# Kernel optimization log

Hardware: AMD Instinct MI355X
Metric: run time of the kernel (lower is better)

## Reference

```python
import jax, jax.numpy as jnp
import numpy as np

B, T, C = 32, 1024, 512
COND_CH = 256            # = L + 4
L = COND_CH - 4          # raw cond length
RES = 64
S = 2 * RES              # kv sequence length
LN_EPS = 1e-5


def _layernorm(x, w, b):
    mu = jnp.mean(x, axis=-1, keepdims=True)
    var = jnp.var(x, axis=-1, keepdims=True)
    return (x - mu) * jax.lax.rsqrt(var + LN_EPS) * w + b


def setup_inputs() -> dict:
    key = jax.random.key(0)
    ks = jax.random.split(key, 12)
    sc = 0.02
    return {
        "x": jax.random.normal(ks[0], (B, T, C), dtype=jnp.float32),
        "cond_emb": jax.random.normal(ks[1], (B, 1, L), dtype=jnp.float32),
        "Wq": sc * jax.random.normal(ks[2], (C, C), dtype=jnp.float32),
        "bq": jnp.zeros((C,), jnp.float32),
        "Wk": sc * jax.random.normal(ks[3], (C, COND_CH), dtype=jnp.float32),
        "bk": jnp.zeros((C,), jnp.float32),
        "Wv": sc * jax.random.normal(ks[4], (C, COND_CH), dtype=jnp.float32),
        "bv": jnp.zeros((C,), jnp.float32),
        "conv_w": sc * jax.random.normal(ks[5], (S, 1, 1), dtype=jnp.float32),
        "conv_b": jnp.zeros((S,), jnp.float32),
        "ln1_w": jnp.ones((C,), jnp.float32),
        "ln1_b": jnp.zeros((C,), jnp.float32),
        "W1": sc * jax.random.normal(ks[6], (2 * C, C), dtype=jnp.float32),
        "b1": jnp.zeros((2 * C,), jnp.float32),
        "W2": sc * jax.random.normal(ks[7], (C, 2 * C), dtype=jnp.float32),
        "b2": jnp.zeros((C,), jnp.float32),
        "ln2_w": jnp.ones((C,), jnp.float32),
        "ln2_b": jnp.zeros((C,), jnp.float32),
    }


def reference(x, cond_emb, Wq, bq, Wk, bk, Wv, bv, conv_w, conv_b,
              ln1_w, ln1_b, W1, b1, W2, b2, ln2_w, ln2_b):
    # conditioner_projection: Conv1d(1, 2*RES, k=1, padding=2, circular)
    # circular pad last dim by 2 on each side -> length L+4 == COND_CH
    pad = jnp.pad(cond_emb, ((0, 0), (0, 0), (2, 2)), mode="wrap")   # [B,1,L+4]
    cond = conv_w.reshape(1, S, 1) * pad + conv_b.reshape(1, S, 1)    # [B,S,L+4]

    q = x @ Wq.T + bq                 # [B,T,C]
    k = cond @ Wk.T + bk              # [B,S,C]
    v = cond @ Wv.T + bv              # [B,S,C]

    scale = 1.0 / jnp.sqrt(jnp.float32(C))
    scores = jnp.einsum("btc,bsc->bts", q, k) * scale   # [B,T,S]
    attn = jax.nn.softmax(scores, axis=-1)
    attn_out = jnp.einsum("bts,bsc->btc", attn, v)       # [B,T,C]

    query = _layernorm(q + attn_out, ln1_w, ln1_b)
    h = jax.nn.gelu(query @ W1.T + b1, approximate=False)
    ff = h @ W2.T + b2
    out = _layernorm(query + ff, ln2_w, ln2_b)
    return out + x
```

## Files before the change

### kernel.cpp

```cpp
#include <hip/hip_runtime.h>
#include <hip/hip_bf16.h>
#include <cstdint>


typedef __attribute__((ext_vector_type(8))) short bf16x8;
typedef __attribute__((ext_vector_type(4))) float f32x4;
typedef __attribute__((ext_vector_type(8))) unsigned short u16x8;

__device__ __forceinline__ float bf2f(unsigned short u) {
  union { unsigned int i; float f; } x; x.i = ((unsigned int)u) << 16; return x.f;
}
__device__ __forceinline__ unsigned short f2bf(float f) {
  unsigned int u = __float_as_uint(f);
  unsigned int r = (u + 0x7FFFu + ((u >> 16) & 1u)) >> 16;
  return (unsigned short)r;
}

__device__ __forceinline__ float wave_sum(float v) {
#pragma unroll
  for (int m = 1; m < 64; m <<= 1) v += __shfl_xor(v, m, 64);
  return v;
}
__device__ __forceinline__ float wave_max(float v) {
#pragma unroll
  for (int m = 1; m < 64; m <<= 1) v = fmaxf(v, __shfl_xor(v, m, 64));
  return v;
}

template <int F32>
__device__ __forceinline__ void stage16(const void* base, size_t eoff,
                                        unsigned short* dst) {
  if (F32) {
    const float* s = (const float*)base + eoff;
    f32x4 a0 = *(const f32x4*)s, a1 = *(const f32x4*)(s + 4);
    u16x8 t;
#pragma unroll
    for (int j = 0; j < 4; ++j) { t[j] = f2bf(a0[j]); t[j + 4] = f2bf(a1[j]); }
    *(u16x8*)dst = t;
  } else {
    *(u16x8*)dst = *(const u16x8*)((const unsigned short*)base + eoff);
  }
}

__global__ __launch_bounds__(256) void prep(
    const float* __restrict__ cond_emb,
    const float* __restrict__ Wk,
    const float* __restrict__ Wv,
    float* __restrict__ Ak, float* __restrict__ Av,
    float* __restrict__ Wks, float* __restrict__ Wvs) {
  const int t = blockIdx.x * 256 + threadIdx.x;
  const int b = t >> 9, c = t & 511;
  const float* ce = cond_emb + b * 252;
  float ak = 0.f, av = 0.f, ks = 0.f, vs = 0.f;
  for (int i = 0; i < 256; ++i) {
    int idx = i - 2; if (idx < 0) idx += 252; if (idx >= 252) idx -= 252;
    float p = ce[idx];
    float wk = Wk[c * 256 + i];
    float wv = Wv[c * 256 + i];
    ak += p * wk; av += p * wv; ks += wk; vs += wv;
  }
  Ak[b * 512 + c] = ak;
  Av[b * 512 + c] = av;
  if (b == 0) { Wks[c] = ks; Wvs[c] = vs; }
}

template <int EPI, int AF32, int BF32>
__global__ __launch_bounds__(256) void gemm_bt(
    const void* __restrict__ Aptr, const void* __restrict__ Bptr,
    const float* __restrict__ bias, unsigned short* __restrict__ Cc,
    int M, int N, int K) {
  __shared__ __align__(16) unsigned short lds_a[128 * 64];
  __shared__ __align__(16) unsigned short lds_b[128 * 64];
  const int nblk = N >> 7;
  const int bm = (int)blockIdx.x / nblk;
  const int bn = (int)blockIdx.x % nblk;
  const int tid = threadIdx.x;
  const int wave = tid >> 6;
  const int lane = tid & 63;
  const int wm = (wave >> 1) << 6;
  const int wn = (wave & 1) << 6;
  const int quad = lane >> 4;
  const int l16 = lane & 15;
  const int srow = lane >> 3;
  const int scol = (lane & 7) << 3;

  f32x4 acc[4][4] = {};

  const size_t abase = (size_t)(bm * 128) * (size_t)K;
  const size_t bbase = (size_t)(bn * 128) * (size_t)K;

  for (int k0 = 0; k0 < K; k0 += 64) {
#pragma unroll
    for (int j = 0; j < 4; ++j) {
      const int rr = wave * 32 + j * 8 + srow;
      stage16<AF32>(Aptr, abase + (size_t)rr * K + (k0 + scol), &lds_a[rr * 64 + scol]);
      stage16<BF32>(Bptr, bbase + (size_t)rr * K + (k0 + scol), &lds_b[rr * 64 + scol]);
    }
    __syncthreads();
#pragma unroll
    for (int kk = 0; kk < 64; kk += 32) {
      bf16x8 af[4], bfr[4];
#pragma unroll
      for (int i = 0; i < 4; ++i)
        af[i] = *(const bf16x8*)&lds_a[(wm + i * 16 + l16) * 64 + kk + quad * 8];
#pragma unroll
      for (int i = 0; i < 4; ++i)
        bfr[i] = *(const bf16x8*)&lds_b[(wn + i * 16 + l16) * 64 + kk + quad * 8];
#pragma unroll
      for (int mi = 0; mi < 4; ++mi)
#pragma unroll
        for (int ni = 0; ni < 4; ++ni)
          acc[mi][ni] = __builtin_amdgcn_mfma_f32_16x16x32_bf16(
              af[mi], bfr[ni], acc[mi][ni], 0, 0, 0);
    }
    __syncthreads();
  }

#pragma unroll
  for (int ni = 0; ni < 4; ++ni) {
    const int col = bn * 128 + wn + ni * 16 + l16;
    const float bsv = bias[col];
#pragma unroll
    for (int mi = 0; mi < 4; ++mi) {
#pragma unroll
      for (int r = 0; r < 4; ++r) {
        const int row = bm * 128 + wm + mi * 16 + quad * 4 + r;
        float v = acc[mi][ni][r] + bsv;
        if (EPI == 1) v = 0.5f * v * (1.0f + erff(v * 0.70710678118654752f));
        Cc[(size_t)row * N + col] = f2bf(v);
      }
    }
  }
}

__global__ __launch_bounds__(256) void attn_ln(
    unsigned short* qbuf,
    const float* __restrict__ Ak, const float* __restrict__ Av,
    const float* __restrict__ Wks, const float* __restrict__ Wvs,
    const float* __restrict__ bk, const float* __restrict__ bv,
    const float* __restrict__ conv_w, const float* __restrict__ conv_b,
    const float* __restrict__ ln1w, const float* __restrict__ ln1b) {
  const int row = (int)((blockIdx.x * 256 + threadIdx.x) >> 6);
  const int lane = threadIdx.x & 63;
  const int b = row >> 10;
  const int c0 = lane << 3;

  const u16x8 qv = *(const u16x8*)(qbuf + (size_t)row * 512 + c0);
  float qf[8];
#pragma unroll
  for (int j = 0; j < 8; ++j) qf[j] = bf2f(qv[j]);

  const f32x4* akp = (const f32x4*)(Ak + b * 512 + c0);
  const f32x4* avp = (const f32x4*)(Av + b * 512 + c0);
  const f32x4* ksp = (const f32x4*)(Wks + c0);
  const f32x4* vsp = (const f32x4*)(Wvs + c0);
  const f32x4* bkp = (const f32x4*)(bk + c0);
  const f32x4* bvp = (const f32x4*)(bv + c0);
  f32x4 ak0 = akp[0], ak1 = akp[1];
  f32x4 av0 = avp[0], av1 = avp[1];
  f32x4 ks0 = ksp[0], ks1 = ksp[1];
  f32x4 vs0 = vsp[0], vs1 = vsp[1];
  f32x4 bk0 = bkp[0], bk1 = bkp[1];
  f32x4 bv0 = bvp[0], bv1 = bvp[1];

  float u = 0.f, w = 0.f, z = 0.f;
#pragma unroll
  for (int j = 0; j < 8; ++j) {
    float a = (j < 4) ? ak0[j] : ak1[j - 4];
    float s = (j < 4) ? ks0[j] : ks1[j - 4];
    float bb = (j < 4) ? bk0[j] : bk1[j - 4];
    u += qf[j] * a;
    w += qf[j] * s;
    z += qf[j] * bb;
  }
  u = wave_sum(u); w = wave_sum(w); z = wave_sum(z);

  const float scale = 0.044194173824159216f;
  const float cw0 = conv_w[lane], cw1 = conv_w[lane + 64];
  const float cb0 = conv_b[lane], cb1 = conv_b[lane + 64];
  float s0 = scale * (cw0 * u + cb0 * w + z);
  float s1 = scale * (cw1 * u + cb1 * w + z);
  float mx = wave_max(fmaxf(s0, s1));
  float e0 = __expf(s0 - mx), e1 = __expf(s1 - mx);
  float se = wave_sum(e0 + e1);
  float sw = wave_sum(e0 * cw0 + e1 * cw1);
  float sb = wave_sum(e0 * cb0 + e1 * cb1);
  float alpha = sw / se, beta = sb / se;

  float y[8], sy = 0.f, syy = 0.f;
#pragma unroll
  for (int j = 0; j < 8; ++j) {
    float a = (j < 4) ? av0[j] : av1[j - 4];
    float s = (j < 4) ? vs0[j] : vs1[j - 4];
    float bb = (j < 4) ? bv0[j] : bv1[j - 4];
    y[j] = qf[j] + alpha * a + beta * s + bb;
    sy += y[j]; syy += y[j] * y[j];
  }
  sy = wave_sum(sy); syy = wave_sum(syy);
  float mu = sy * (1.0f / 512.0f);
  float var = syy * (1.0f / 512.0f) - mu * mu;
  float rstd = rsqrtf(var + 1e-5f);

  const f32x4* wp = (const f32x4*)(ln1w + c0);
  const f32x4* bp = (const f32x4*)(ln1b + c0);
  f32x4 w0 = wp[0], w1 = wp[1];
  f32x4 b0 = bp[0], b1 = bp[1];
  u16x8 outv;
#pragma unroll
  for (int j = 0; j < 8; ++j) {
    float ww = (j < 4) ? w0[j] : w1[j - 4];
    float bb = (j < 4) ? b0[j] : b1[j - 4];
    outv[j] = f2bf((y[j] - mu) * rstd * ww + bb);
  }
  *(u16x8*)(qbuf + (size_t)row * 512 + c0) = outv;
}

__global__ __launch_bounds__(256) void ln2_res(
    const unsigned short* __restrict__ query,
    const unsigned short* __restrict__ ff,
    const float* __restrict__ x,
    const float* __restrict__ ln2w, const float* __restrict__ ln2b,
    float* __restrict__ out) {
  const int row = (int)((blockIdx.x * 256 + threadIdx.x) >> 6);
  const int lane = threadIdx.x & 63;
  const int c0 = lane << 3;
  const size_t off = (size_t)row * 512 + c0;

  const u16x8 qv = *(const u16x8*)(query + off);
  const u16x8 fv = *(const u16x8*)(ff + off);
  const f32x4* xp = (const f32x4*)(x + off);
  f32x4 x0 = xp[0], x1 = xp[1];
  float y[8], sy = 0.f, syy = 0.f;
#pragma unroll
  for (int j = 0; j < 8; ++j) {
    y[j] = bf2f(qv[j]) + bf2f(fv[j]);
    sy += y[j]; syy += y[j] * y[j];
  }
  sy = wave_sum(sy); syy = wave_sum(syy);
  float mu = sy * (1.0f / 512.0f);
  float var = syy * (1.0f / 512.0f) - mu * mu;
  float rstd = rsqrtf(var + 1e-5f);

  const f32x4* wp = (const f32x4*)(ln2w + c0);
  const f32x4* bp = (const f32x4*)(ln2b + c0);
  f32x4 w0 = wp[0], w1 = wp[1];
  f32x4 b0 = bp[0], b1 = bp[1];
  f32x4 o0, o1;
#pragma unroll
  for (int j = 0; j < 4; ++j) {
    o0[j] = (y[j] - mu) * rstd * w0[j] + b0[j] + x0[j];
    o1[j] = (y[j + 4] - mu) * rstd * w1[j] + b1[j] + x1[j];
  }
  *(f32x4*)(out + off) = o0;
  *(f32x4*)(out + off + 4) = o1;
}


extern "C" void kernel_launch(void* const* d_in, const int* in_sizes, int n_in,
                              void* d_out, int out_size, void* d_ws, size_t ws_size,
                              hipStream_t stream) {
  const float* x        = (const float*)d_in[0];
  const float* cond_emb = (const float*)d_in[1];
  const float* Wq       = (const float*)d_in[2];
  const float* bq       = (const float*)d_in[3];
  const float* Wk       = (const float*)d_in[4];
  const float* bk       = (const float*)d_in[5];
  const float* Wv       = (const float*)d_in[6];
  const float* bv       = (const float*)d_in[7];
  const float* conv_w   = (const float*)d_in[8];
  const float* conv_b   = (const float*)d_in[9];
  const float* ln1w     = (const float*)d_in[10];
  const float* ln1b     = (const float*)d_in[11];
  const float* W1       = (const float*)d_in[12];
  const float* b1       = (const float*)d_in[13];
  const float* W2       = (const float*)d_in[14];
  const float* b2       = (const float*)d_in[15];
  const float* ln2w     = (const float*)d_in[16];
  const float* ln2b     = (const float*)d_in[17];
  float* out = (float*)d_out;

  const int M = 32768;

  char* ws = (char*)d_ws;
  float* Ak  = (float*)(ws);
  float* Av  = (float*)(ws + 65536);
  float* Wks = (float*)(ws + 131072);
  float* Wvs = (float*)(ws + 135168);
  const size_t qoff = (size_t)1 << 20;
  const size_t qbytes = (size_t)M * 512 * 2;
  unsigned short* qbuf = (unsigned short*)(ws + qoff);

  int nc = 1;
  while (nc < 256) {
    size_t need = qoff + qbytes + (size_t)(M / nc) * 3072;
    if (need <= ws_size) break;
    nc <<= 1;
  }
  const int Mc = M / nc;
  unsigned short* hbuf  = (unsigned short*)(ws + qoff + qbytes);
  unsigned short* ffbuf = (unsigned short*)(ws + qoff + qbytes + (size_t)Mc * 2048);

  prep<<<64, 256, 0, stream>>>(cond_emb, Wk, Wv, Ak, Av, Wks, Wvs);

  gemm_bt<0, 1, 1><<<(M / 128) * (512 / 128), 256, 0, stream>>>(
      (const void*)x, (const void*)Wq, bq, qbuf, M, 512, 512);

  attn_ln<<<M / 4, 256, 0, stream>>>(qbuf, Ak, Av, Wks, Wvs, bk, bv,
                                     conv_w, conv_b, ln1w, ln1b);

  for (int c = 0; c < nc; ++c) {
    const size_t roff = (size_t)c * Mc;
    gemm_bt<1, 0, 1><<<(Mc / 128) * (1024 / 128), 256, 0, stream>>>(
        (const void*)(qbuf + roff * 512), (const void*)W1, b1, hbuf, Mc, 1024, 512);
    gemm_bt<0, 0, 1><<<(Mc / 128) * (512 / 128), 256, 0, stream>>>(
        (const void*)hbuf, (const void*)W2, b2, ffbuf, Mc, 512, 1024);
    ln2_res<<<Mc / 4, 256, 0, stream>>>(qbuf + roff * 512, ffbuf, x + roff * 512,
                                        ln2w, ln2b, out + roff * 512);
  }
}
```

Before: 468.7 us.

## Pre-convert weights and x to bf16, stage GEMM tiles via async global-to-LDS loads

Adds a conversion kernel that casts Wq, W1, W2 (and x when workspace allows) to bf16 once per call. The GEMMs then stage bf16 tiles with global_load_lds direct-to-LDS copies instead of register round-trips with per-element fp32-to-bf16 conversion. The prep kernel is also vectorised with float4 weight loads. This removes repeated weight conversion in every GEMM tile, but adds extra passes over x and the weights plus more workspace use.

```diff
diff --git a/kernel.cpp b/kernel.cpp
--- a/kernel.cpp
+++ b/kernel.cpp
@@ -6,6 +6,7 @@
 typedef __attribute__((ext_vector_type(8))) short bf16x8;
 typedef __attribute__((ext_vector_type(4))) float f32x4;
 typedef __attribute__((ext_vector_type(8))) unsigned short u16x8;
+typedef __attribute__((ext_vector_type(4))) unsigned short u16x4;
 
 __device__ __forceinline__ float bf2f(unsigned short u) {
   union { unsigned int i; float f; } x; x.i = ((unsigned int)u) << 16; return x.f;
@@ -27,19 +28,20 @@
   return v;
 }
 
-template <int F32>
-__device__ __forceinline__ void stage16(const void* base, size_t eoff,
-                                        unsigned short* dst) {
-  if (F32) {
-    const float* s = (const float*)base + eoff;
-    f32x4 a0 = *(const f32x4*)s, a1 = *(const f32x4*)(s + 4);
-    u16x8 t;
-#pragma unroll
-    for (int j = 0; j < 4; ++j) { t[j] = f2bf(a0[j]); t[j + 4] = f2bf(a1[j]); }
-    *(u16x8*)dst = t;
-  } else {
-    *(u16x8*)dst = *(const u16x8*)((const unsigned short*)base + eoff);
-  }
+__device__ __forceinline__ void async16(const void* g, void* l) {
+  __builtin_amdgcn_global_load_lds(
+      (const __attribute__((address_space(1))) void*)g,
+      (__attribute__((address_space(3))) void*)l, 16, 0, 0);
+}
+
+__global__ __launch_bounds__(256) void cvt(
+    const float* __restrict__ in, unsigned short* __restrict__ o) {
+  const int i = (blockIdx.x * 256 + threadIdx.x) * 4;
+  f32x4 v = *(const f32x4*)(in + i);
+  u16x4 t;
+#pragma unroll
+  for (int j = 0; j < 4; ++j) t[j] = f2bf(v[j]);
+  *(u16x4*)(o + i) = t;
 }
 
 __global__ __launch_bounds__(256) void prep(
@@ -52,21 +54,24 @@
   const int b = t >> 9, c = t & 511;
   const float* ce = cond_emb + b * 252;
   float ak = 0.f, av = 0.f, ks = 0.f, vs = 0.f;
-  for (int i = 0; i < 256; ++i) {
-    int idx = i - 2; if (idx < 0) idx += 252; if (idx >= 252) idx -= 252;
-    float p = ce[idx];
-    float wk = Wk[c * 256 + i];
-    float wv = Wv[c * 256 + i];
-    ak += p * wk; av += p * wv; ks += wk; vs += wv;
+  for (int i = 0; i < 256; i += 4) {
+    f32x4 wk = *(const f32x4*)(Wk + c * 256 + i);
+    f32x4 wv = *(const f32x4*)(Wv + c * 256 + i);
+#pragma unroll
+    for (int j = 0; j < 4; ++j) {
+      int idx = i + j - 2; if (idx < 0) idx += 252; if (idx >= 252) idx -= 252;
+      float p = ce[idx];
+      ak += p * wk[j]; av += p * wv[j]; ks += wk[j]; vs += wv[j];
+    }
   }
   Ak[b * 512 + c] = ak;
   Av[b * 512 + c] = av;
   if (b == 0) { Wks[c] = ks; Wvs[c] = vs; }
 }
 
-template <int EPI, int AF32, int BF32>
+template <int EPI, int AF32>
 __global__ __launch_bounds__(256) void gemm_bt(
-    const void* __restrict__ Aptr, const void* __restrict__ Bptr,
+    const void* __restrict__ Aptr, const unsigned short* __restrict__ Bm,
     const float* __restrict__ bias, unsigned short* __restrict__ Cc,
     int M, int N, int K) {
   __shared__ __align__(16) unsigned short lds_a[128 * 64];
@@ -92,9 +97,19 @@
   for (int k0 = 0; k0 < K; k0 += 64) {
 #pragma unroll
     for (int j = 0; j < 4; ++j) {
-      const int rr = wave * 32 + j * 8 + srow;
-      stage16<AF32>(Aptr, abase + (size_t)rr * K + (k0 + scol), &lds_a[rr * 64 + scol]);
-      stage16<BF32>(Bptr, bbase + (size_t)rr * K + (k0 + scol), &lds_b[rr * 64 + scol]);
+      const int r = wave * 32 + j * 8;
+      if (AF32) {
+        const float* src = (const float*)Aptr + abase + (size_t)(r + srow) * K + (k0 + scol);
+        f32x4 a0 = *(const f32x4*)src, a1 = *(const f32x4*)(src + 4);
+        u16x8 tv;
+#pragma unroll
+        for (int jj = 0; jj < 4; ++jj) { tv[jj] = f2bf(a0[jj]); tv[jj + 4] = f2bf(a1[jj]); }
+        *(u16x8*)&lds_a[(r + srow) * 64 + scol] = tv;
+      } else {
+        async16((const unsigned short*)Aptr + abase + (size_t)(r + srow) * K + (k0 + scol),
+                &lds_a[r * 64]);
+      }
+      async16(Bm + bbase + (size_t)(r + srow) * K + (k0 + scol), &lds_b[r * 64]);
     }
     __syncthreads();
 #pragma unroll
@@ -169,9 +184,7 @@
     float a = (j < 4) ? ak0[j] : ak1[j - 4];
     float s = (j < 4) ? ks0[j] : ks1[j - 4];
     float bb = (j < 4) ? bk0[j] : bk1[j - 4];
-    u += qf[j] * a;
-    w += qf[j] * s;
-    z += qf[j] * bb;
+    u += qf[j] * a; w += qf[j] * s; z += qf[j] * bb;
   }
   u = wave_sum(u); w = wave_sum(w); z = wave_sum(z);
 
@@ -286,34 +299,46 @@
   float* Av  = (float*)(ws + 65536);
   float* Wks = (float*)(ws + 131072);
   float* Wvs = (float*)(ws + 135168);
-  const size_t qoff = (size_t)1 << 20;
-  const size_t qbytes = (size_t)M * 512 * 2;
-  unsigned short* qbuf = (unsigned short*)(ws + qoff);
+  size_t off = 147456;
+  unsigned short* Wqb = (unsigned short*)(ws + off); off += (size_t)512 * 512 * 2;
+  unsigned short* W1b = (unsigned short*)(ws + off); off += (size_t)1024 * 512 * 2;
+  unsigned short* W2b = (unsigned short*)(ws + off); off += (size_t)512 * 1024 * 2;
+  unsigned short* qbuf = (unsigned short*)(ws + off); off += (size_t)M * 512 * 2;
+
+  const size_t xb_bytes = (size_t)M * 512 * 2;
+  const int use_xb = (ws_size >= off + xb_bytes + (size_t)(M / 8) * 3072) ? 1 : 0;
+  unsigned short* xb = (unsigned short*)(ws + off);
+  if (use_xb) off += xb_bytes;
 
   int nc = 1;
-  while (nc < 256) {
-    size_t need = qoff + qbytes + (size_t)(M / nc) * 3072;
-    if (need <= ws_size) break;
-    nc <<= 1;
-  }
+  while (nc < 256 && off + (size_t)(M / nc) * 3072 > ws_size) nc <<= 1;
   const int Mc = M / nc;
-  unsigned short* hbuf  = (unsigned short*)(ws + qoff + qbytes);
-  unsigned short* ffbuf = (unsigned short*)(ws + qoff + qbytes + (size_t)Mc * 2048);
+  unsigned short* hbuf  = (unsigned short*)(ws + off);
+  unsigned short* ffbuf = (unsigned short*)(ws + off + (size_t)Mc * 2048);
+
+  cvt<<<256, 256, 0, stream>>>(Wq, Wqb);
+  cvt<<<512, 256, 0, stream>>>(W1, W1b);
+  cvt<<<512, 256, 0, stream>>>(W2, W2b);
+  if (use_xb) cvt<<<16384, 256, 0, stream>>>(x, xb);
 
   prep<<<64, 256, 0, stream>>>(cond_emb, Wk, Wv, Ak, Av, Wks, Wvs);
 
-  gemm_bt<0, 1, 1><<<(M / 128) * (512 / 128), 256, 0, stream>>>(
-      (const void*)x, (const void*)Wq, bq, qbuf, M, 512, 512);
+  if (use_xb)
+    gemm_bt<0, 0><<<(M / 128) * (512 / 128), 256, 0, stream>>>(
+        (const void*)xb, Wqb, bq, qbuf, M, 512, 512);
+  else
+    gemm_bt<0, 1><<<(M / 128) * (512 / 128), 256, 0, stream>>>(
+        (const void*)x, Wqb, bq, qbuf, M, 512, 512);
 
   attn_ln<<<M / 4, 256, 0, stream>>>(qbuf, Ak, Av, Wks, Wvs, bk, bv,
                                      conv_w, conv_b, ln1w, ln1b);
 
   for (int c = 0; c < nc; ++c) {
     const size_t roff = (size_t)c * Mc;
-    gemm_bt<1, 0, 1><<<(Mc / 128) * (1024 / 128), 256, 0, stream>>>(
-        (const void*)(qbuf + roff * 512), (const void*)W1, b1, hbuf, Mc, 1024, 512);
-    gemm_bt<0, 0, 1><<<(Mc / 128) * (512 / 128), 256, 0, stream>>>(
-        (const void*)hbuf, (const void*)W2, b2, ffbuf, Mc, 512, 1024);
+    gemm_bt<1, 0><<<(Mc / 128) * (1024 / 128), 256, 0, stream>>>(
+        (const void*)(qbuf + roff * 512), W1b, b1, hbuf, Mc, 1024, 512);
+    gemm_bt<0, 0><<<(Mc / 128) * (512 / 128), 256, 0, stream>>>(
+        (const void*)hbuf, W2b, b2, ffbuf, Mc, 512, 1024);
     ln2_res<<<Mc / 4, 256, 0, stream>>>(qbuf + roff * 512, ffbuf, x + roff * 512,
                                         ln2w, ln2b, out + roff * 512);
   }
```

New measurement: 391.1 us. -16.6%, faster.
